# Kernel tuning notes

Hardware: AMD Instinct MI355X
Metric: run time of the kernel (lower is better)

Reference implementation:

```python
import jax, jax.numpy as jnp
import numpy as np


def setup_inputs() -> dict:
    key = jax.random.key(0)
    k1, k2 = jax.random.split(key)
    N, K, D = 65536, 512, 512
    x = jax.random.normal(k1, (N, D), dtype=jnp.float32)
    centroids = jax.random.normal(k2, (K, D), dtype=jnp.float32)
    return {"x": x, "centroids": centroids}


def reference(x, centroids):
    # Squared pairwise distances via matmul expansion (same math as
    # sum((x[:,None,:] - c[None,:,:])**2, axis=2), without the [N,K,D] blowup):
    x_sq = jnp.sum(x * x, axis=1, keepdims=True)            # [N, 1]
    c_sq = jnp.sum(centroids * centroids, axis=1)            # [K]
    d2 = x_sq + c_sq[None, :] - 2.0 * (x @ centroids.T)      # [N, K]
    q = 1.0 / (1.0 + d2)                                     # Student-t kernel, alpha=1
    q = q / jnp.sum(q, axis=1, keepdims=True)                # row normalize
    return q
```

## Files before the change

### kernel.cpp

```cpp
#include <hip/hip_runtime.h>
#include <stdint.h>


#define D 512
#define K 512
#define BM 64
#define BK 64
#define NCHUNK (D / BK)
#define THREADS 512
#define ESTRIDE 516

typedef __attribute__((ext_vector_type(8))) short short8;
typedef __attribute__((ext_vector_type(4))) float floatx4;

__device__ __forceinline__ uint16_t f2bf(float f) {
  uint32_t u = __float_as_uint(f);
  u += 0x7FFFu + ((u >> 16) & 1u);
  return (uint16_t)(u >> 16);
}

__device__ __forceinline__ uint4 pack8(float4 v0, float4 v1) {
  uint4 pk;
  pk.x = (uint32_t)f2bf(v0.x) | ((uint32_t)f2bf(v0.y) << 16);
  pk.y = (uint32_t)f2bf(v0.z) | ((uint32_t)f2bf(v0.w) << 16);
  pk.z = (uint32_t)f2bf(v1.x) | ((uint32_t)f2bf(v1.y) << 16);
  pk.w = (uint32_t)f2bf(v1.z) | ((uint32_t)f2bf(v1.w) << 16);
  return pk;
}

__device__ __forceinline__ float sq8(float4 v0, float4 v1) {
  return v0.x*v0.x + v0.y*v0.y + v0.z*v0.z + v0.w*v0.w
       + v1.x*v1.x + v1.y*v1.y + v1.z*v1.z + v1.w*v1.w;
}

__global__ __launch_bounds__(64)
void prep_kernel(const float* __restrict__ cent, float* __restrict__ csq,
                 uint16_t* __restrict__ bbf) {
  const int row  = blockIdx.x;
  const int lane = threadIdx.x;
  const float4* src = (const float4*)(cent + (size_t)row * D + lane * 8);
  float4 v0 = src[0];
  float4 v1 = src[1];
  float ss = sq8(v0, v1);
  uint4 pk = pack8(v0, v1);
  const int c = lane >> 3;
  const int g = lane & 7;
  const int slot = ((c * 2 + (g >> 2)) * 512 + row) * 4 + (g & 3);
  *(uint4*)(bbf + (size_t)slot * 8) = pk;
  #pragma unroll
  for (int m = 1; m < 64; m <<= 1) ss += __shfl_xor(ss, m);
  if (lane == 0) csq[row] = ss;
}

__global__ __launch_bounds__(THREADS, 4)
void cluster_main(const float* __restrict__ x, const uint16_t* __restrict__ bbf,
                  const float* __restrict__ csq, float* __restrict__ out) {
  __shared__ __align__(16) char smem[32 * ESTRIDE * 4];
  __shared__ float lxsq[BM];
  __shared__ float lrow[BM];
  uint16_t* const lA = (uint16_t*)smem;
  float* const ebuf  = (float*)smem;

  const int tid  = threadIdx.x;
  const int wave = tid >> 6;
  const int lane = tid & 63;
  const int p    = lane & 15;
  const int quad = lane >> 4;
  const int row0 = blockIdx.x * BM;

  if (tid < BM) lrow[tid] = 0.f;

  const int ar = tid >> 3;
  const int ag = tid & 7;
  const int adst = (ar * 8 + (ag ^ (ar & 7))) * 8;
  const float* xp = x + (size_t)(row0 + ar) * D + ag * 8;
  float xacc = 0.f;

  const uint16_t* const bl = bbf + ((wave * 64 + p) * 32 + quad * 8);

  floatx4 acc[4][4];
  #pragma unroll
  for (int mi = 0; mi < 4; ++mi)
    #pragma unroll
    for (int ni = 0; ni < 4; ++ni)
      acc[mi][ni] = (floatx4){0.f, 0.f, 0.f, 0.f};

  {
    float4 pv0 = *(const float4*)xp;
    float4 pv1 = *(const float4*)(xp + 4);
    xp += BK;
    xacc += sq8(pv0, pv1);
    *(uint4*)(lA + adst) = pack8(pv0, pv1);
  }
  float4 nv0 = *(const float4*)xp;
  float4 nv1 = *(const float4*)(xp + 4);
  xp += BK;
  asm volatile("s_waitcnt lgkmcnt(0)" ::: "memory");
  __builtin_amdgcn_s_barrier();
  asm volatile("" ::: "memory");

  #pragma unroll
  for (int c = 0; c < NCHUNK; ++c) {
    const uint16_t* const Acur = lA + (c & 1) * (BM * BK);
    uint16_t* const Anxt = (uint16_t*)lA + ((c & 1) ^ 1) * (BM * BK);
    const uint16_t* const bc = bl + c * 32768;

    short8 b0[4];
    #pragma unroll
    for (int ni = 0; ni < 4; ++ni)
      b0[ni] = *(const short8*)(bc + ni * 512);

    if (c < NCHUNK - 1) {
      xacc += sq8(nv0, nv1);
      *(uint4*)(Anxt + adst) = pack8(nv0, nv1);
    }

    short8 b1[4];
    #pragma unroll
    for (int ni = 0; ni < 4; ++ni)
      b1[ni] = *(const short8*)(bc + 16384 + ni * 512);
    if (c < NCHUNK - 2) {
      nv0 = *(const float4*)xp;
      nv1 = *(const float4*)(xp + 4);
      xp += BK;
    }

    #pragma unroll
    for (int mi = 0; mi < 4; ++mi) {
      const int r = mi * 16 + p;
      short8 af = *(const short8*)(Acur + (r * 8 + (quad ^ (r & 7))) * 8);
      #pragma unroll
      for (int ni = 0; ni < 4; ++ni)
        acc[mi][ni] = __builtin_amdgcn_mfma_f32_16x16x32_bf16(
            af, b0[ni], acc[mi][ni], 0, 0, 0);
    }
    #pragma unroll
    for (int mi = 0; mi < 4; ++mi) {
      const int r = mi * 16 + p;
      short8 af = *(const short8*)(Acur + (r * 8 + ((4 + quad) ^ (r & 7))) * 8);
      #pragma unroll
      for (int ni = 0; ni < 4; ++ni)
        acc[mi][ni] = __builtin_amdgcn_mfma_f32_16x16x32_bf16(
            af, b1[ni], acc[mi][ni], 0, 0, 0);
    }

    if (c < NCHUNK - 1) {
      asm volatile("s_waitcnt lgkmcnt(0)" ::: "memory");
      __builtin_amdgcn_s_barrier();
      asm volatile("" ::: "memory");
    }
  }

  xacc += __shfl_xor(xacc, 1);
  xacc += __shfl_xor(xacc, 2);
  xacc += __shfl_xor(xacc, 4);
  if (ag == 0) lxsq[ar] = xacc;
  __syncthreads();

  float xs[4][4];
  #pragma unroll
  for (int mi = 0; mi < 4; ++mi)
    #pragma unroll
    for (int rr = 0; rr < 4; ++rr)
      xs[mi][rr] = lxsq[mi * 16 + quad * 4 + rr];
  float cs[4];
  #pragma unroll
  for (int ni = 0; ni < 4; ++ni)
    cs[ni] = csq[wave * 64 + ni * 16 + p];

  float rp[4][4];
  #pragma unroll
  for (int mi = 0; mi < 4; ++mi)
    #pragma unroll
    for (int rr = 0; rr < 4; ++rr)
      rp[mi][rr] = 0.f;

  #pragma unroll
  for (int mi = 0; mi < 4; ++mi)
    #pragma unroll
    for (int ni = 0; ni < 4; ++ni)
      #pragma unroll
      for (int rr = 0; rr < 4; ++rr) {
        const float d = 1.0f + xs[mi][rr] + cs[ni] - 2.0f * acc[mi][ni][rr];
        const float q = __builtin_amdgcn_rcpf(d);
        acc[mi][ni][rr] = q;
        rp[mi][rr] += q;
      }

  #pragma unroll
  for (int mi = 0; mi < 4; ++mi)
    #pragma unroll
    for (int rr = 0; rr < 4; ++rr) {
      float v = rp[mi][rr];
      v += __shfl_xor(v, 1);
      v += __shfl_xor(v, 2);
      v += __shfl_xor(v, 4);
      v += __shfl_xor(v, 8);
      if (p == 0) atomicAdd(&lrow[mi * 16 + quad * 4 + rr], v);
    }
  __syncthreads();

  float inv[4][4];
  #pragma unroll
  for (int mi = 0; mi < 4; ++mi)
    #pragma unroll
    for (int rr = 0; rr < 4; ++rr)
      inv[mi][rr] = __builtin_amdgcn_rcpf(lrow[mi * 16 + quad * 4 + rr]);

  #pragma unroll
  for (int pass = 0; pass < 2; ++pass) {
    if (pass) __syncthreads();
    #pragma unroll
    for (int h = 0; h < 2; ++h) {
      const int mi = pass * 2 + h;
      #pragma unroll
      for (int ni = 0; ni < 4; ++ni)
        #pragma unroll
        for (int rr = 0; rr < 4; ++rr)
          ebuf[(h * 16 + quad * 4 + rr) * ESTRIDE + wave * 64 + ni * 16 + p] =
              acc[mi][ni][rr] * inv[mi][rr];
    }
    __syncthreads();
    #pragma unroll
    for (int j = 0; j < 8; ++j) {
      const int idx = j * 512 + tid;
      const int r  = idx >> 7;
      const int c4 = idx & 127;
      const float4 v = *(const float4*)&ebuf[r * ESTRIDE + c4 * 4];
      *(float4*)(out + (size_t)(row0 + pass * 32 + r) * K + c4 * 4) = v;
    }
  }
}

extern "C" void kernel_launch(void* const* d_in, const int* in_sizes, int n_in,
                              void* d_out, int out_size, void* d_ws, size_t ws_size,
                              hipStream_t stream) {
  const float* x    = (const float*)d_in[0];
  const float* cent = (const float*)d_in[1];
  float* out = (float*)d_out;

  float*    csq = (float*)d_ws;
  uint16_t* bbf = (uint16_t*)((char*)d_ws + 2048);

  const int N = in_sizes[0] / D;
  prep_kernel<<<K, 64, 0, stream>>>(cent, csq, bbf);
  cluster_main<<<N / BM, THREADS, 0, stream>>>(x, bbf, csq, out);
}
```

Measured before the change: 257.1 us.

## Stage full bf16 A tile in LDS once and pipeline B fragment loads

The kernel now loads the whole 64x512 row tile of x up front, converts it to bf16 and stores it in LDS in one go. This replaces the double-buffered 64-wide K chunks and removes the per-chunk barriers from the MFMA loop. B fragments are re-laid out per 32-wide k-step and prefetched in an even/odd register ping-pong. The epilogue writes 16-row slices so it fits in the new 64 KB LDS buffer. The cost is a much larger LDS footprint, which can lower occupancy below the requested 4 blocks per CU, and the global loads of x no longer overlap with the MFMA work.

```diff
diff --git a/kernel.cpp b/kernel.cpp
--- a/kernel.cpp
+++ b/kernel.cpp
@@ -5,8 +5,7 @@
 #define D 512
 #define K 512
 #define BM 64
-#define BK 64
-#define NCHUNK (D / BK)
+#define NKS (D / 32)
 #define THREADS 512
 #define ESTRIDE 516
 
@@ -43,9 +42,9 @@
   float4 v1 = src[1];
   float ss = sq8(v0, v1);
   uint4 pk = pack8(v0, v1);
-  const int c = lane >> 3;
-  const int g = lane & 7;
-  const int slot = ((c * 2 + (g >> 2)) * 512 + row) * 4 + (g & 3);
+  const int ks = lane >> 2;
+  const int qd = lane & 3;
+  const int slot = (ks * 512 + row) * 4 + qd;
   *(uint4*)(bbf + (size_t)slot * 8) = pk;
   #pragma unroll
   for (int m = 1; m < 64; m <<= 1) ss += __shfl_xor(ss, m);
@@ -55,7 +54,7 @@
 __global__ __launch_bounds__(THREADS, 4)
 void cluster_main(const float* __restrict__ x, const uint16_t* __restrict__ bbf,
                   const float* __restrict__ csq, float* __restrict__ out) {
-  __shared__ __align__(16) char smem[32 * ESTRIDE * 4];
+  __shared__ __align__(16) char smem[BM * D * 2];
   __shared__ float lxsq[BM];
   __shared__ float lrow[BM];
   uint16_t* const lA = (uint16_t*)smem;
@@ -72,90 +71,81 @@
 
   const int ar = tid >> 3;
   const int ag = tid & 7;
-  const int adst = (ar * 8 + (ag ^ (ar & 7))) * 8;
-  const float* xp = x + (size_t)(row0 + ar) * D + ag * 8;
+  const float* xrow = x + (size_t)(row0 + ar) * D + ag * 8;
   float xacc = 0.f;
-
-  const uint16_t* const bl = bbf + ((wave * 64 + p) * 32 + quad * 8);
-
-  floatx4 acc[4][4];
-  #pragma unroll
-  for (int mi = 0; mi < 4; ++mi)
-    #pragma unroll
-    for (int ni = 0; ni < 4; ++ni)
-      acc[mi][ni] = (floatx4){0.f, 0.f, 0.f, 0.f};
-
-  {
-    float4 pv0 = *(const float4*)xp;
-    float4 pv1 = *(const float4*)(xp + 4);
-    xp += BK;
-    xacc += sq8(pv0, pv1);
-    *(uint4*)(lA + adst) = pack8(pv0, pv1);
+  #pragma unroll
+  for (int h = 0; h < 2; ++h) {
+    float4 v[8];
+    #pragma unroll
+    for (int j = 0; j < 4; ++j) {
+      v[2*j]   = *(const float4*)(xrow + (h*4 + j) * 64);
+      v[2*j+1] = *(const float4*)(xrow + (h*4 + j) * 64 + 4);
+    }
+    #pragma unroll
+    for (int j = 0; j < 4; ++j) {
+      xacc += sq8(v[2*j], v[2*j+1]);
+      const int gi = (h*4 + j) * 8 + ag;
+      *(uint4*)(lA + (size_t)ar * 512 + ((gi ^ (ar & 7)) * 8)) =
+          pack8(v[2*j], v[2*j+1]);
+    }
   }
-  float4 nv0 = *(const float4*)xp;
-  float4 nv1 = *(const float4*)(xp + 4);
-  xp += BK;
-  asm volatile("s_waitcnt lgkmcnt(0)" ::: "memory");
-  __builtin_amdgcn_s_barrier();
-  asm volatile("" ::: "memory");
-
-  #pragma unroll
-  for (int c = 0; c < NCHUNK; ++c) {
-    const uint16_t* const Acur = lA + (c & 1) * (BM * BK);
-    uint16_t* const Anxt = (uint16_t*)lA + ((c & 1) ^ 1) * (BM * BK);
-    const uint16_t* const bc = bl + c * 32768;
-
-    short8 b0[4];
-    #pragma unroll
-    for (int ni = 0; ni < 4; ++ni)
-      b0[ni] = *(const short8*)(bc + ni * 512);
-
-    if (c < NCHUNK - 1) {
-      xacc += sq8(nv0, nv1);
-      *(uint4*)(Anxt + adst) = pack8(nv0, nv1);
-    }
-
-    short8 b1[4];
-    #pragma unroll
-    for (int ni = 0; ni < 4; ++ni)
-      b1[ni] = *(const short8*)(bc + 16384 + ni * 512);
-    if (c < NCHUNK - 2) {
-      nv0 = *(const float4*)xp;
-      nv1 = *(const float4*)(xp + 4);
-      xp += BK;
-    }
-
-    #pragma unroll
-    for (int mi = 0; mi < 4; ++mi) {
-      const int r = mi * 16 + p;
-      short8 af = *(const short8*)(Acur + (r * 8 + (quad ^ (r & 7))) * 8);
-      #pragma unroll
-      for (int ni = 0; ni < 4; ++ni)
-        acc[mi][ni] = __builtin_amdgcn_mfma_f32_16x16x32_bf16(
-            af, b0[ni], acc[mi][ni], 0, 0, 0);
-    }
-    #pragma unroll
-    for (int mi = 0; mi < 4; ++mi) {
-      const int r = mi * 16 + p;
-      short8 af = *(const short8*)(Acur + (r * 8 + ((4 + quad) ^ (r & 7))) * 8);
-      #pragma unroll
-      for (int ni = 0; ni < 4; ++ni)
-        acc[mi][ni] = __builtin_amdgcn_mfma_f32_16x16x32_bf16(
-            af, b1[ni], acc[mi][ni], 0, 0, 0);
-    }
-
-    if (c < NCHUNK - 1) {
-      asm volatile("s_waitcnt lgkmcnt(0)" ::: "memory");
-      __builtin_amdgcn_s_barrier();
-      asm volatile("" ::: "memory");
-    }
-  }
-
   xacc += __shfl_xor(xacc, 1);
   xacc += __shfl_xor(xacc, 2);
   xacc += __shfl_xor(xacc, 4);
   if (ag == 0) lxsq[ar] = xacc;
+
+  floatx4 acc[4][4];
+  #pragma unroll
+  for (int mi = 0; mi < 4; ++mi)
+    #pragma unroll
+    for (int ni = 0; ni < 4; ++ni)
+      acc[mi][ni] = (floatx4){0.f, 0.f, 0.f, 0.f};
+
   __syncthreads();
+
+  const uint16_t* const bl = bbf + ((wave * 64 + p) * 32 + quad * 8);
+
+  short8 bE[4], bO[4];
+  #pragma unroll
+  for (int ni = 0; ni < 4; ++ni)
+    bE[ni] = *(const short8*)(bl + ni * 512);
+
+  #pragma unroll
+  for (int s = 0; s < 8; ++s) {
+    const int ks0 = 2 * s, ks1 = 2 * s + 1;
+
+    #pragma unroll
+    for (int ni = 0; ni < 4; ++ni)
+      bO[ni] = *(const short8*)(bl + ks1 * 16384 + ni * 512);
+
+    #pragma unroll
+    for (int mi = 0; mi < 4; ++mi) {
+      const int r = mi * 16 + p;
+      short8 af = *(const short8*)(
+          lA + (size_t)r * 512 + ((((ks0 * 4 + quad) ^ (r & 7))) * 8));
+      #pragma unroll
+      for (int ni = 0; ni < 4; ++ni)
+        acc[mi][ni] = __builtin_amdgcn_mfma_f32_16x16x32_bf16(
+            af, bE[ni], acc[mi][ni], 0, 0, 0);
+    }
+
+    if (s < 7) {
+      #pragma unroll
+      for (int ni = 0; ni < 4; ++ni)
+        bE[ni] = *(const short8*)(bl + (ks0 + 2) * 16384 + ni * 512);
+    }
+
+    #pragma unroll
+    for (int mi = 0; mi < 4; ++mi) {
+      const int r = mi * 16 + p;
+      short8 af = *(const short8*)(
+          lA + (size_t)r * 512 + ((((ks1 * 4 + quad) ^ (r & 7))) * 8));
+      #pragma unroll
+      for (int ni = 0; ni < 4; ++ni)
+        acc[mi][ni] = __builtin_amdgcn_mfma_f32_16x16x32_bf16(
+            af, bO[ni], acc[mi][ni], 0, 0, 0);
+    }
+  }
 
   float xs[4][4];
   #pragma unroll
@@ -208,26 +198,22 @@
       inv[mi][rr] = __builtin_amdgcn_rcpf(lrow[mi * 16 + quad * 4 + rr]);
 
   #pragma unroll
-  for (int pass = 0; pass < 2; ++pass) {
-    if (pass) __syncthreads();
-    #pragma unroll
-    for (int h = 0; h < 2; ++h) {
-      const int mi = pass * 2 + h;
-      #pragma unroll
-      for (int ni = 0; ni < 4; ++ni)
-        #pragma unroll
-        for (int rr = 0; rr < 4; ++rr)
-          ebuf[(h * 16 + quad * 4 + rr) * ESTRIDE + wave * 64 + ni * 16 + p] =
-              acc[mi][ni][rr] * inv[mi][rr];
-    }
+  for (int s = 0; s < 4; ++s) {
+    if (s) __syncthreads();
+    #pragma unroll
+    for (int ni = 0; ni < 4; ++ni)
+      #pragma unroll
+      for (int rr = 0; rr < 4; ++rr)
+        ebuf[(quad * 4 + rr) * ESTRIDE + wave * 64 + ni * 16 + p] =
+            acc[s][ni][rr] * inv[s][rr];
     __syncthreads();
     #pragma unroll
-    for (int j = 0; j < 8; ++j) {
+    for (int j = 0; j < 4; ++j) {
       const int idx = j * 512 + tid;
       const int r  = idx >> 7;
       const int c4 = idx & 127;
       const float4 v = *(const float4*)&ebuf[r * ESTRIDE + c4 * 4];
-      *(float4*)(out + (size_t)(row0 + pass * 32 + r) * K + c4 * 4) = v;
+      *(float4*)(out + (size_t)(row0 + s * 16 + r) * K + c4 * 4) = v;
     }
   }
 }
```

Result: slower. 269.0 us (+4.6%).

## Halve row tile, widen per-wave column span, store output directly

Applied to the files above, without the earlier changes.

Shrinks the row tile from 64 to 32 and the block from 512 to 256 threads. Each wave now covers 128 centroid columns with a 2x8 MFMA accumulator grid, and the prep kernel writes the bf16 centroids in a matching layout. The epilogue no longer stages results through LDS; it issues direct nontemporal scalar stores from registers. This aims to free LDS, raise occupancy and drop the staging barriers, but it doubles the number of blocks re-reading the full centroid matrix and gives less coalesced output stores.

```diff
diff --git a/kernel.cpp b/kernel.cpp
--- a/kernel.cpp
+++ b/kernel.cpp
@@ -4,14 +4,19 @@
 
 #define D 512
 #define K 512
-#define BM 64
+#define BM 32
 #define BK 64
 #define NCHUNK (D / BK)
-#define THREADS 512
-#define ESTRIDE 516
+#define THREADS 256
 
 typedef __attribute__((ext_vector_type(8))) short short8;
 typedef __attribute__((ext_vector_type(4))) float floatx4;
+
+#define BARRIER() do {                                      \
+    asm volatile("s_waitcnt lgkmcnt(0)" ::: "memory");      \
+    __builtin_amdgcn_s_barrier();                           \
+    asm volatile("" ::: "memory");                          \
+  } while (0)
 
 __device__ __forceinline__ uint16_t f2bf(float f) {
   uint32_t u = __float_as_uint(f);
@@ -43,9 +48,9 @@
   float4 v1 = src[1];
   float ss = sq8(v0, v1);
   uint4 pk = pack8(v0, v1);
-  const int c = lane >> 3;
-  const int g = lane & 7;
-  const int slot = ((c * 2 + (g >> 2)) * 512 + row) * 4 + (g & 3);
+  const int ks = lane >> 2;
+  const int qd = lane & 3;
+  const int slot = (ks * 512 + row) * 4 + qd;
   *(uint4*)(bbf + (size_t)slot * 8) = pk;
   #pragma unroll
   for (int m = 1; m < 64; m <<= 1) ss += __shfl_xor(ss, m);
@@ -55,14 +60,12 @@
 __global__ __launch_bounds__(THREADS, 4)
 void cluster_main(const float* __restrict__ x, const uint16_t* __restrict__ bbf,
                   const float* __restrict__ csq, float* __restrict__ out) {
-  __shared__ __align__(16) char smem[32 * ESTRIDE * 4];
+  __shared__ __align__(16) uint16_t lA[2][BM * BK];
   __shared__ float lxsq[BM];
   __shared__ float lrow[BM];
-  uint16_t* const lA = (uint16_t*)smem;
-  float* const ebuf  = (float*)smem;
 
   const int tid  = threadIdx.x;
-  const int wave = tid >> 6;
+  const int w    = tid >> 6;
   const int lane = tid & 63;
   const int p    = lane & 15;
   const int quad = lane >> 4;
@@ -72,83 +75,105 @@
 
   const int ar = tid >> 3;
   const int ag = tid & 7;
-  const int adst = (ar * 8 + (ag ^ (ar & 7))) * 8;
+  const int adst = ar * 64 + ((ag ^ (ar & 7)) * 8);
   const float* xp = x + (size_t)(row0 + ar) * D + ag * 8;
   float xacc = 0.f;
 
-  const uint16_t* const bl = bbf + ((wave * 64 + p) * 32 + quad * 8);
-
-  floatx4 acc[4][4];
-  #pragma unroll
-  for (int mi = 0; mi < 4; ++mi)
-    #pragma unroll
-    for (int ni = 0; ni < 4; ++ni)
+  const uint16_t* const bl = bbf + (((size_t)(w * 128 + p) * 4 + quad) * 8);
+
+  floatx4 acc[2][8];
+  #pragma unroll
+  for (int mi = 0; mi < 2; ++mi)
+    #pragma unroll
+    for (int ni = 0; ni < 8; ++ni)
       acc[mi][ni] = (floatx4){0.f, 0.f, 0.f, 0.f};
 
   {
-    float4 pv0 = *(const float4*)xp;
-    float4 pv1 = *(const float4*)(xp + 4);
+    float4 a0 = *(const float4*)xp;
+    float4 a1 = *(const float4*)(xp + 4);
     xp += BK;
-    xacc += sq8(pv0, pv1);
-    *(uint4*)(lA + adst) = pack8(pv0, pv1);
+    xacc += sq8(a0, a1);
+    *(uint4*)&lA[0][adst] = pack8(a0, a1);
   }
   float4 nv0 = *(const float4*)xp;
   float4 nv1 = *(const float4*)(xp + 4);
   xp += BK;
-  asm volatile("s_waitcnt lgkmcnt(0)" ::: "memory");
-  __builtin_amdgcn_s_barrier();
-  asm volatile("" ::: "memory");
+  BARRIER();
 
   #pragma unroll
   for (int c = 0; c < NCHUNK; ++c) {
-    const uint16_t* const Acur = lA + (c & 1) * (BM * BK);
-    uint16_t* const Anxt = (uint16_t*)lA + ((c & 1) ^ 1) * (BM * BK);
-    const uint16_t* const bc = bl + c * 32768;
-
-    short8 b0[4];
-    #pragma unroll
-    for (int ni = 0; ni < 4; ++ni)
-      b0[ni] = *(const short8*)(bc + ni * 512);
+    const int cur = c & 1;
+    const uint16_t* const bc0 = bl + (size_t)c * 32768;
+    const uint16_t* const bc1 = bc0 + 16384;
+
+    short8 b0[4], b1[4];
+
+    #pragma unroll
+    for (int ni = 0; ni < 4; ++ni)
+      b0[ni] = *(const short8*)(bc0 + ni * 512);
 
     if (c < NCHUNK - 1) {
       xacc += sq8(nv0, nv1);
-      *(uint4*)(Anxt + adst) = pack8(nv0, nv1);
-    }
-
-    short8 b1[4];
-    #pragma unroll
-    for (int ni = 0; ni < 4; ++ni)
-      b1[ni] = *(const short8*)(bc + 16384 + ni * 512);
+      *(uint4*)&lA[cur ^ 1][adst] = pack8(nv0, nv1);
+    }
+
+    #pragma unroll
+    for (int ni = 0; ni < 4; ++ni)
+      b1[ni] = *(const short8*)(bc0 + 2048 + ni * 512);
     if (c < NCHUNK - 2) {
       nv0 = *(const float4*)xp;
       nv1 = *(const float4*)(xp + 4);
       xp += BK;
     }
 
-    #pragma unroll
-    for (int mi = 0; mi < 4; ++mi) {
+    short8 af0[2];
+    #pragma unroll
+    for (int mi = 0; mi < 2; ++mi) {
       const int r = mi * 16 + p;
-      short8 af = *(const short8*)(Acur + (r * 8 + (quad ^ (r & 7))) * 8);
+      af0[mi] = *(const short8*)&lA[cur][r * 64 + ((quad ^ (r & 7)) * 8)];
+    }
+    #pragma unroll
+    for (int mi = 0; mi < 2; ++mi)
       #pragma unroll
       for (int ni = 0; ni < 4; ++ni)
         acc[mi][ni] = __builtin_amdgcn_mfma_f32_16x16x32_bf16(
-            af, b0[ni], acc[mi][ni], 0, 0, 0);
-    }
-    #pragma unroll
-    for (int mi = 0; mi < 4; ++mi) {
+            af0[mi], b0[ni], acc[mi][ni], 0, 0, 0);
+
+    #pragma unroll
+    for (int ni = 0; ni < 4; ++ni)
+      b0[ni] = *(const short8*)(bc1 + ni * 512);
+
+    #pragma unroll
+    for (int mi = 0; mi < 2; ++mi)
+      #pragma unroll
+      for (int ni = 0; ni < 4; ++ni)
+        acc[mi][ni + 4] = __builtin_amdgcn_mfma_f32_16x16x32_bf16(
+            af0[mi], b1[ni], acc[mi][ni + 4], 0, 0, 0);
+
+    #pragma unroll
+    for (int ni = 0; ni < 4; ++ni)
+      b1[ni] = *(const short8*)(bc1 + 2048 + ni * 512);
+
+    short8 af1[2];
+    #pragma unroll
+    for (int mi = 0; mi < 2; ++mi) {
       const int r = mi * 16 + p;
-      short8 af = *(const short8*)(Acur + (r * 8 + ((4 + quad) ^ (r & 7))) * 8);
+      af1[mi] = *(const short8*)&lA[cur][r * 64 + (((4 + quad) ^ (r & 7)) * 8)];
+    }
+    #pragma unroll
+    for (int mi = 0; mi < 2; ++mi)
       #pragma unroll
       for (int ni = 0; ni < 4; ++ni)
         acc[mi][ni] = __builtin_amdgcn_mfma_f32_16x16x32_bf16(
-            af, b1[ni], acc[mi][ni], 0, 0, 0);
-    }
-
-    if (c < NCHUNK - 1) {
-      asm volatile("s_waitcnt lgkmcnt(0)" ::: "memory");
-      __builtin_amdgcn_s_barrier();
-      asm volatile("" ::: "memory");
-    }
+            af1[mi], b0[ni], acc[mi][ni], 0, 0, 0);
+    #pragma unroll
+    for (int mi = 0; mi < 2; ++mi)
+      #pragma unroll
+      for (int ni = 0; ni < 4; ++ni)
+        acc[mi][ni + 4] = __builtin_amdgcn_mfma_f32_16x16x32_bf16(
+            af1[mi], b1[ni], acc[mi][ni + 4], 0, 0, 0);
+
+    if (c < NCHUNK - 1) BARRIER();
   }
 
   xacc += __shfl_xor(xacc, 1);
@@ -157,38 +182,35 @@
   if (ag == 0) lxsq[ar] = xacc;
   __syncthreads();
 
-  float xs[4][4];
-  #pragma unroll
-  for (int mi = 0; mi < 4; ++mi)
-    #pragma unroll
-    for (int rr = 0; rr < 4; ++rr)
-      xs[mi][rr] = lxsq[mi * 16 + quad * 4 + rr];
-  float cs[4];
-  #pragma unroll
-  for (int ni = 0; ni < 4; ++ni)
-    cs[ni] = csq[wave * 64 + ni * 16 + p];
-
-  float rp[4][4];
-  #pragma unroll
-  for (int mi = 0; mi < 4; ++mi)
+  float cs[8];
+  #pragma unroll
+  for (int ni = 0; ni < 8; ++ni)
+    cs[ni] = csq[w * 128 + ni * 16 + p];
+
+  float rp[2][4];
+  #pragma unroll
+  for (int mi = 0; mi < 2; ++mi)
     #pragma unroll
     for (int rr = 0; rr < 4; ++rr)
       rp[mi][rr] = 0.f;
 
   #pragma unroll
-  for (int mi = 0; mi < 4; ++mi)
-    #pragma unroll
-    for (int ni = 0; ni < 4; ++ni)
-      #pragma unroll
-      for (int rr = 0; rr < 4; ++rr) {
-        const float d = 1.0f + xs[mi][rr] + cs[ni] - 2.0f * acc[mi][ni][rr];
+  for (int mi = 0; mi < 2; ++mi) {
+    #pragma unroll
+    for (int rr = 0; rr < 4; ++rr) {
+      const float xsv = lxsq[mi * 16 + quad * 4 + rr];
+      #pragma unroll
+      for (int ni = 0; ni < 8; ++ni) {
+        const float d = 1.0f + xsv + cs[ni] - 2.0f * acc[mi][ni][rr];
         const float q = __builtin_amdgcn_rcpf(d);
         acc[mi][ni][rr] = q;
         rp[mi][rr] += q;
       }
-
-  #pragma unroll
-  for (int mi = 0; mi < 4; ++mi)
+    }
+  }
+
+  #pragma unroll
+  for (int mi = 0; mi < 2; ++mi)
     #pragma unroll
     for (int rr = 0; rr < 4; ++rr) {
       float v = rp[mi][rr];
@@ -200,34 +222,16 @@
     }
   __syncthreads();
 
-  float inv[4][4];
-  #pragma unroll
-  for (int mi = 0; mi < 4; ++mi)
-    #pragma unroll
-    for (int rr = 0; rr < 4; ++rr)
-      inv[mi][rr] = __builtin_amdgcn_rcpf(lrow[mi * 16 + quad * 4 + rr]);
-
-  #pragma unroll
-  for (int pass = 0; pass < 2; ++pass) {
-    if (pass) __syncthreads();
-    #pragma unroll
-    for (int h = 0; h < 2; ++h) {
-      const int mi = pass * 2 + h;
-      #pragma unroll
-      for (int ni = 0; ni < 4; ++ni)
-        #pragma unroll
-        for (int rr = 0; rr < 4; ++rr)
-          ebuf[(h * 16 + quad * 4 + rr) * ESTRIDE + wave * 64 + ni * 16 + p] =
-              acc[mi][ni][rr] * inv[mi][rr];
-    }
-    __syncthreads();
-    #pragma unroll
-    for (int j = 0; j < 8; ++j) {
-      const int idx = j * 512 + tid;
-      const int r  = idx >> 7;
-      const int c4 = idx & 127;
-      const float4 v = *(const float4*)&ebuf[r * ESTRIDE + c4 * 4];
-      *(float4*)(out + (size_t)(row0 + pass * 32 + r) * K + c4 * 4) = v;
+  #pragma unroll
+  for (int mi = 0; mi < 2; ++mi) {
+    #pragma unroll
+    for (int rr = 0; rr < 4; ++rr) {
+      const int row = mi * 16 + quad * 4 + rr;
+      const float inv = __builtin_amdgcn_rcpf(lrow[row]);
+      float* orow = out + (size_t)(row0 + row) * K + w * 128 + p;
+      #pragma unroll
+      for (int ni = 0; ni < 8; ++ni)
+        __builtin_nontemporal_store(acc[mi][ni][rr] * inv, orow + ni * 16);
     }
   }
 }
```

Result: slower. 293.6 us (+14.2%).
